# Kernel tuning notes

Measured on AMD Instinct MI355X. Metric: run time of the kernel, lower is better.

Reference implementation:

```python
import jax, jax.numpy as jnp
import numpy as np

N_NODES = 50000
N_EDGES = 640000
HIDDEN = 128
EDGE_DIM = 32


def _init_linear(key, fan_in, fan_out):
    kw, kb = jax.random.split(key)
    bound = 1.0 / np.sqrt(fan_in)
    W = jax.random.uniform(kw, (fan_in, fan_out), jnp.float32, -bound, bound)
    b = jax.random.uniform(kb, (fan_out,), jnp.float32, -bound, bound)
    return W, b


def setup_inputs() -> dict:
    key = jax.random.key(0)
    ks = jax.random.split(key, 10)
    node_features = jax.random.normal(ks[0], (N_NODES, HIDDEN), jnp.float32)
    edge_index = jax.random.randint(ks[1], (2, N_EDGES), 0, N_NODES, jnp.int64)
    edge_features = jax.random.normal(ks[2], (N_EDGES, EDGE_DIM), jnp.float32)
    coordination = jax.random.uniform(ks[3], (N_NODES,), jnp.float32)
    msg_in = 2 * HIDDEN + EDGE_DIM + 2
    upd_in = 2 * HIDDEN + 1
    mW1, mb1 = _init_linear(ks[4], msg_in, HIDDEN)
    mW2, mb2 = _init_linear(ks[5], HIDDEN, HIDDEN)
    uW1, ub1 = _init_linear(ks[6], upd_in, HIDDEN)
    uW2, ub2 = _init_linear(ks[7], HIDDEN, HIDDEN)
    ln_gamma = jnp.ones((HIDDEN,), jnp.float32)
    ln_beta = jnp.zeros((HIDDEN,), jnp.float32)
    return {
        "node_features": node_features,
        "edge_index": edge_index,
        "edge_features": edge_features,
        "coordination": coordination,
        "mW1": mW1, "mb1": mb1, "mW2": mW2, "mb2": mb2,
        "uW1": uW1, "ub1": ub1, "uW2": uW2, "ub2": ub2,
        "ln_gamma": ln_gamma, "ln_beta": ln_beta,
    }


def _layernorm(x, gamma, beta, eps=1e-5):
    mu = jnp.mean(x, axis=-1, keepdims=True)
    var = jnp.mean(jnp.square(x - mu), axis=-1, keepdims=True)
    return (x - mu) * jax.lax.rsqrt(var + eps) * gamma + beta


def reference(node_features, edge_index, edge_features, coordination,
              mW1, mb1, mW2, mb2, uW1, ub1, uW2, ub2, ln_gamma, ln_beta):
    n_nodes = node_features.shape[0]
    src, dst = edge_index[0], edge_index[1]
    # edge_input: [E, 2H + edge_dim + 2]
    edge_input = jnp.concatenate([
        node_features[src],
        node_features[dst],
        edge_features,
        coordination[src][:, None],
        coordination[dst][:, None],
    ], axis=-1)
    h = jax.nn.silu(edge_input @ mW1 + mb1)
    messages = h @ mW2 + mb2  # [E, H]
    aggregated = jax.ops.segment_sum(messages, dst, num_segments=n_nodes)  # [N, H]
    update_input = jnp.concatenate([
        node_features, aggregated, coordination[:, None]
    ], axis=-1)  # [N, 2H+1]
    u = jax.nn.silu(update_input @ uW1 + ub1)
    upd = u @ uW2 + ub2
    return _layernorm(node_features + upd, ln_gamma, ln_beta)
```

## Files before the change

### kernel.cpp

```cpp
#include <hip/hip_runtime.h>

#define NN 50000
#define NE 640000
#define HID 128


typedef __attribute__((ext_vector_type(8))) short bf8;
typedef __attribute__((ext_vector_type(4))) float f4;

#define MFMA(a, b, c) __builtin_amdgcn_mfma_f32_16x16x32_bf16(a, b, c, 0, 0, 0)

__device__ __forceinline__ short f2bf(float f) {
    union { float f; unsigned u; } v; v.f = f;
    unsigned r = v.u + 0x7FFFu + ((v.u >> 16) & 1u);
    return (short)(r >> 16);
}
__device__ __forceinline__ float bf2f(short s) {
    union { unsigned u; float f; } v; v.u = ((unsigned)(unsigned short)s) << 16;
    return v.f;
}
__device__ __forceinline__ float silu(float x) {
    return x * __builtin_amdgcn_rcpf(1.f + __expf(-x));
}

__global__ void pack_weights_kernel(const float* __restrict__ mW1, const float* __restrict__ mb1,
                                    const float* __restrict__ mW2,
                                    const float* __restrict__ uW1, const float* __restrict__ uW2,
                                    short* __restrict__ Wpre, short* __restrict__ W1e,
                                    short* __restrict__ W2p, short* __restrict__ U1p,
                                    short* __restrict__ U2p,
                                    float* __restrict__ Waux, float* __restrict__ Baux) {
    const int stride = gridDim.x * blockDim.x;
    const int idx = blockIdx.x * blockDim.x + threadIdx.x;
    for (int t = idx; t < 256 * 128; t += stride) {
        int cc = t / 128, k = t % 128;
        float v = (cc < 128) ? mW1[k * 128 + cc] : mW1[(128 + k) * 128 + (cc - 128)];
        Wpre[t] = f2bf(v);
    }
    for (int t = idx; t < 128 * 32; t += stride) {
        int c = t / 32, k = t % 32;
        W1e[t] = f2bf(mW1[(256 + k) * 128 + c]);
    }
    for (int t = idx; t < 128 * 128; t += stride)
        W2p[t] = f2bf(mW2[(t % 128) * 128 + (t / 128)]);
    for (int t = idx; t < 128 * 288; t += stride) {
        int n = t / 288, k = t % 288;
        U1p[t] = (k < 257) ? f2bf(uW1[k * 128 + n]) : (short)0;
    }
    for (int t = idx; t < 128 * 128; t += stride)
        U2p[t] = f2bf(uW2[(t % 128) * 128 + (t / 128)]);
    for (int t = idx; t < 256; t += stride) {
        Waux[t] = (t < 128) ? mW1[288 * 128 + t] : mW1[289 * 128 + (t - 128)];
        Baux[t] = (t < 128) ? 0.f : mb1[t - 128];
    }
}

__global__ __launch_bounds__(256, 3)
void node_pre_kernel(const float* __restrict__ nf, const float* __restrict__ coord,
                     const short* __restrict__ Wpre, const float* __restrict__ Waux,
                     const float* __restrict__ Baux, short* __restrict__ Ppre) {
    __shared__ short SH[64 * 264];
    __shared__ float scoord[64];
    short* A = SH;
    short* P = SH;
    const int tid = threadIdx.x;
    const int nbase = blockIdx.x * 64;

    {
        const int r = tid >> 2, q = tid & 3;
        const int node = nbase + r;
        short* Ar = A + r * 136 + q * 32;
        if (node < NN) {
            const float* p = nf + (long)node * HID + q * 32;
#pragma unroll
            for (int j = 0; j < 4; ++j) {
                f4 v0 = *(const f4*)(p + j * 8), v1 = *(const f4*)(p + j * 8 + 4);
                bf8 w = { f2bf(v0[0]), f2bf(v0[1]), f2bf(v0[2]), f2bf(v0[3]),
                          f2bf(v1[0]), f2bf(v1[1]), f2bf(v1[2]), f2bf(v1[3]) };
                *(bf8*)(Ar + j * 8) = w;
            }
            if (q == 0) scoord[r] = coord[node];
        } else {
            bf8 z = {};
#pragma unroll
            for (int j = 0; j < 4; ++j) *(bf8*)(Ar + j * 8) = z;
            if (q == 0) scoord[r] = 0.f;
        }
    }
    __syncthreads();

    const int lane = tid & 63, wv = tid >> 6;
    const int g = lane >> 4, i16 = lane & 15, wc = wv * 64;

    f4 acc[4][4] = {};
#pragma unroll
    for (int ks = 0; ks < 4; ++ks) {
        const int kb = ks * 32 + g * 8;
        bf8 b[4];
#pragma unroll
        for (int n = 0; n < 4; ++n)
            b[n] = *(const bf8*)(Wpre + (wc + n * 16 + i16) * 128 + kb);
#pragma unroll
        for (int m = 0; m < 4; ++m) {
            bf8 a = *(const bf8*)(A + (m * 16 + i16) * 136 + kb);
#pragma unroll
            for (int n = 0; n < 4; ++n) acc[m][n] = MFMA(a, b[n], acc[m][n]);
        }
    }
    __syncthreads();

#pragma unroll
    for (int n = 0; n < 4; ++n) {
        const int cc = wc + n * 16 + i16;
        const float wa = Waux[cc], ba = Baux[cc];
#pragma unroll
        for (int m = 0; m < 4; ++m)
#pragma unroll
            for (int i = 0; i < 4; ++i) {
                const int row = m * 16 + g * 4 + i;
                P[row * 264 + cc] = f2bf(acc[m][n][i] + scoord[row] * wa + ba);
            }
    }
    __syncthreads();

    {
        const int r = tid >> 2, q = tid & 3;
        const int node = nbase + r;
        if (node < NN) {
#pragma unroll
            for (int j = 0; j < 8; ++j)
                *(bf8*)(Ppre + (long)node * 256 + q * 64 + j * 8) =
                    *(const bf8*)(P + r * 264 + q * 64 + j * 8);
        }
    }
}

__global__ void hist_kernel(const int* __restrict__ ei, int* __restrict__ hist) {
    const int stride = gridDim.x * blockDim.x;
    for (int e = blockIdx.x * blockDim.x + threadIdx.x; e < NE; e += stride)
        atomicAdd(&hist[ei[NE + e]], 1);
}

__global__ void scan1_kernel(const int* __restrict__ hist, int* __restrict__ pos,
                             int* __restrict__ csum) {
    __shared__ int s[256];
    const int b = blockIdx.x, t = threadIdx.x;
    const int idx = b * 200 + t;
    int v = (t < 200) ? hist[idx] : 0;
    s[t] = v;
    __syncthreads();
    for (int d = 1; d < 256; d <<= 1) {
        int x = (t >= d) ? s[t - d] : 0;
        __syncthreads();
        s[t] += x;
        __syncthreads();
    }
    if (t < 200) pos[idx] = s[t] - v;
    if (t == 255) csum[b] = s[255];
}

__global__ void scan2_kernel(int* __restrict__ csum) {
    __shared__ int s[256];
    const int t = threadIdx.x;
    int v = (t < 250) ? csum[t] : 0;
    s[t] = v;
    __syncthreads();
    for (int d = 1; d < 256; d <<= 1) {
        int x = (t >= d) ? s[t - d] : 0;
        __syncthreads();
        s[t] += x;
        __syncthreads();
    }
    if (t < 250) csum[t] = s[t] - v;
}

__global__ void scan3_kernel(int* __restrict__ pos, const int* __restrict__ csum) {
    const int b = blockIdx.x, t = threadIdx.x;
    if (t < 200) pos[b * 200 + t] += csum[b];
}

__global__ void scatter_kernel(const int* __restrict__ ei, int* __restrict__ pos,
                               int* __restrict__ perm) {
    const int stride = gridDim.x * blockDim.x;
    for (int e = blockIdx.x * blockDim.x + threadIdx.x; e < NE; e += stride) {
        const int d = ei[NE + e];
        const int p = atomicAdd(&pos[d], 1);
        perm[p] = e;
    }
}

__global__ __launch_bounds__(256, 4)
void edge_kernel(const int* __restrict__ ei, const float* __restrict__ ef,
                 const int* __restrict__ perm, const short* __restrict__ Ppre,
                 const short* __restrict__ W1e, const short* __restrict__ W2p,
                 const float* __restrict__ mb2, float* __restrict__ agg) {
    constexpr int LDEF = 40, LDH = 136, LDM = 132;
    __shared__ float R[64 * 132];
    __shared__ int sdst[64], ssrc[64];
    short* Aef = (short*)R;
    short* H = (short*)R;
    float* M = R;

    const int tid = threadIdx.x;
    const int bid = blockIdx.x;
    const int ebase = ((bid & 7) * 1250 + (bid >> 3)) * 64;

    {
        const int r = tid >> 2, q = tid & 3;
        const int e = perm[ebase + r];
        if (q == 0) { ssrc[r] = ei[e]; sdst[r] = ei[NE + e]; }
        const float* pe = ef + (long)e * 32 + q * 8;
        f4 v0 = *(const f4*)pe, v1 = *(const f4*)(pe + 4);
        bf8 w = { f2bf(v0[0]), f2bf(v0[1]), f2bf(v0[2]), f2bf(v0[3]),
                  f2bf(v1[0]), f2bf(v1[1]), f2bf(v1[2]), f2bf(v1[3]) };
        *(bf8*)(Aef + r * LDEF + q * 8) = w;
    }
    __syncthreads();

    const int lane = tid & 63, wv = tid >> 6;
    const int g = lane >> 4, i16 = lane & 15, wc = wv * 32;

    f4 acc[4][2] = {};
    {
        bf8 b0 = *(const bf8*)(W1e + (wc + i16) * 32 + g * 8);
        bf8 b1 = *(const bf8*)(W1e + (wc + 16 + i16) * 32 + g * 8);
#pragma unroll
        for (int m = 0; m < 4; ++m) {
            bf8 a = *(const bf8*)(Aef + (m * 16 + i16) * LDEF + g * 8);
            acc[m][0] = MFMA(a, b0, acc[m][0]);
            acc[m][1] = MFMA(a, b1, acc[m][1]);
        }
    }
    __syncthreads();

#pragma unroll
    for (int m = 0; m < 4; ++m)
#pragma unroll
        for (int n = 0; n < 2; ++n)
#pragma unroll
            for (int i = 0; i < 4; ++i)
                H[(m * 16 + g * 4 + i) * LDH + wc + n * 16 + i16] = f2bf(acc[m][n][i]);
    __syncthreads();

    {
        const int r = tid >> 2, q = tid & 3;
        const short* p1 = Ppre + (long)ssrc[r] * 256 + q * 32;
        const short* p2 = Ppre + (long)sdst[r] * 256 + 128 + q * 32;
        bf8 a1[4], a2[4];
#pragma unroll
        for (int j = 0; j < 4; ++j) { a1[j] = *(const bf8*)(p1 + j * 8); }
#pragma unroll
        for (int j = 0; j < 4; ++j) { a2[j] = *(const bf8*)(p2 + j * 8); }
        short* Hr = H + r * LDH + q * 32;
#pragma unroll
        for (int j = 0; j < 4; ++j)
#pragma unroll
            for (int t = 0; t < 8; ++t) {
                float x = bf2f(Hr[j * 8 + t]) + bf2f(a1[j][t]) + bf2f(a2[j][t]);
                Hr[j * 8 + t] = f2bf(silu(x));
            }
    }
    __syncthreads();

    f4 acc2[4][2] = {};
#pragma unroll
    for (int ks = 0; ks < 4; ++ks) {
        const int kb = ks * 32 + g * 8;
        bf8 b0 = *(const bf8*)(W2p + (wc + i16) * 128 + kb);
        bf8 b1 = *(const bf8*)(W2p + (wc + 16 + i16) * 128 + kb);
#pragma unroll
        for (int m = 0; m < 4; ++m) {
            bf8 a = *(const bf8*)(H + (m * 16 + i16) * LDH + kb);
            acc2[m][0] = MFMA(a, b0, acc2[m][0]);
            acc2[m][1] = MFMA(a, b1, acc2[m][1]);
        }
    }
    __syncthreads();

    {
        const float c0 = mb2[wc + i16], c1 = mb2[wc + 16 + i16];
#pragma unroll
        for (int m = 0; m < 4; ++m)
#pragma unroll
            for (int n = 0; n < 2; ++n)
#pragma unroll
                for (int i = 0; i < 4; ++i)
                    M[(m * 16 + g * 4 + i) * LDM + wc + n * 16 + i16] =
                        acc2[m][n][i] + (n ? c1 : c0);
    }
    __syncthreads();

    {
        const int col = tid >> 1, half = tid & 1;
        const int r0 = half * 32, r1 = r0 + 32;
        float run = 0.f;
#pragma unroll
        for (int r = r0; r < r1; ++r) {
            run += M[r * LDM + col];
            const bool last = (r == r1 - 1) || (sdst[r + 1] != sdst[r]);
            if (last) {
                atomicAdd(agg + (long)sdst[r] * HID + col, run);
                run = 0.f;
            }
        }
    }
}

__global__ __launch_bounds__(256, 4)
void node_kernel(const float* __restrict__ nf, const float* __restrict__ agg,
                 const float* __restrict__ coord,
                 const short* __restrict__ U1p, const float* __restrict__ ub1,
                 const short* __restrict__ U2p, const float* __restrict__ ub2,
                 const float* __restrict__ gamma, const float* __restrict__ beta,
                 float* __restrict__ out) {
    constexpr int K1 = 288, LDA = 296, LDH = 136, LDX = 132;
    __shared__ short SH[64 * LDA];
    short* A = SH;
    short* H = SH;
    float* X = (float*)SH;

    const int tid = threadIdx.x;
    const int nbase = blockIdx.x * 64;

    {
        const int r = tid >> 2, q = tid & 3;
        const int node = nbase + r;
        short* Ar = A + r * LDA;
        bf8 z = {};
        if (node < NN) {
            const float* pn = nf + (long)node * HID + q * 32;
            const float* pa = agg + (long)node * HID + q * 32;
#pragma unroll
            for (int j = 0; j < 4; ++j) {
                f4 v0 = *(const f4*)(pn + j * 8), v1 = *(const f4*)(pn + j * 8 + 4);
                bf8 w = { f2bf(v0[0]), f2bf(v0[1]), f2bf(v0[2]), f2bf(v0[3]),
                          f2bf(v1[0]), f2bf(v1[1]), f2bf(v1[2]), f2bf(v1[3]) };
                *(bf8*)(Ar + q * 32 + j * 8) = w;
            }
#pragma unroll
            for (int j = 0; j < 4; ++j) {
                f4 v0 = *(const f4*)(pa + j * 8), v1 = *(const f4*)(pa + j * 8 + 4);
                bf8 w = { f2bf(v0[0]), f2bf(v0[1]), f2bf(v0[2]), f2bf(v0[3]),
                          f2bf(v1[0]), f2bf(v1[1]), f2bf(v1[2]), f2bf(v1[3]) };
                *(bf8*)(Ar + 128 + q * 32 + j * 8) = w;
            }
            *(bf8*)(Ar + 256 + q * 8) = z;
            if (q == 0) Ar[256] = f2bf(coord[node]);
        } else {
#pragma unroll
            for (int j = 0; j < 4; ++j) {
                *(bf8*)(Ar + q * 32 + j * 8) = z;
                *(bf8*)(Ar + 128 + q * 32 + j * 8) = z;
            }
            *(bf8*)(Ar + 256 + q * 8) = z;
        }
    }
    __syncthreads();

    const int lane = tid & 63, wv = tid >> 6;
    const int g = lane >> 4, i16 = lane & 15, wc = wv * 32;

    f4 acc[4][2] = {};
#pragma unroll
    for (int ks = 0; ks < K1 / 32; ++ks) {
        const int kb = ks * 32 + g * 8;
        bf8 b0 = *(const bf8*)(U1p + (wc + i16) * K1 + kb);
        bf8 b1 = *(const bf8*)(U1p + (wc + 16 + i16) * K1 + kb);
#pragma unroll
        for (int m = 0; m < 4; ++m) {
            bf8 a = *(const bf8*)(A + (m * 16 + i16) * LDA + kb);
            acc[m][0] = MFMA(a, b0, acc[m][0]);
            acc[m][1] = MFMA(a, b1, acc[m][1]);
        }
    }
    __syncthreads();

    {
        const float c0 = ub1[wc + i16], c1 = ub1[wc + 16 + i16];
#pragma unroll
        for (int m = 0; m < 4; ++m)
#pragma unroll
            for (int n = 0; n < 2; ++n)
#pragma unroll
                for (int i = 0; i < 4; ++i) {
                    float x = acc[m][n][i] + (n ? c1 : c0);
                    H[(m * 16 + g * 4 + i) * LDH + wc + n * 16 + i16] = f2bf(silu(x));
                }
    }
    __syncthreads();

    f4 acc2[4][2] = {};
#pragma unroll
    for (int ks = 0; ks < 4; ++ks) {
        const int kb = ks * 32 + g * 8;
        bf8 b0 = *(const bf8*)(U2p + (wc + i16) * 128 + kb);
        bf8 b1 = *(const bf8*)(U2p + (wc + 16 + i16) * 128 + kb);
#pragma unroll
        for (int m = 0; m < 4; ++m) {
            bf8 a = *(const bf8*)(H + (m * 16 + i16) * LDH + kb);
            acc2[m][0] = MFMA(a, b0, acc2[m][0]);
            acc2[m][1] = MFMA(a, b1, acc2[m][1]);
        }
    }
    __syncthreads();

    {
        const float c0 = ub2[wc + i16], c1 = ub2[wc + 16 + i16];
#pragma unroll
        for (int m = 0; m < 4; ++m)
#pragma unroll
            for (int n = 0; n < 2; ++n)
#pragma unroll
                for (int i = 0; i < 4; ++i) {
                    const int row = m * 16 + g * 4 + i;
                    const int node = nbase + row;
                    const int col = wc + n * 16 + i16;
                    float v = acc2[m][n][i] + (n ? c1 : c0);
                    float base = (node < NN) ? nf[(long)node * HID + col] : 0.f;
                    X[row * LDX + col] = base + v;
                }
    }
    __syncthreads();

    {
        const int r = tid >> 2, q = tid & 3;
        const int node = nbase + r;
        float s = 0.f;
#pragma unroll
        for (int j = 0; j < 32; ++j) s += X[r * LDX + q * 32 + j];
        s += __shfl_xor(s, 1);
        s += __shfl_xor(s, 2);
        const float mu = s * (1.f / 128.f);
        float vv = 0.f;
#pragma unroll
        for (int j = 0; j < 32; ++j) {
            float d = X[r * LDX + q * 32 + j] - mu;
            vv += d * d;
        }
        vv += __shfl_xor(vv, 1);
        vv += __shfl_xor(vv, 2);
        const float rstd = rsqrtf(vv * (1.f / 128.f) + 1e-5f);
        if (node < NN) {
#pragma unroll
            for (int j = 0; j < 32; ++j) {
                const int c = q * 32 + j;
                out[(long)node * HID + c] = (X[r * LDX + c] - mu) * rstd * gamma[c] + beta[c];
            }
        }
    }
}

extern "C" void kernel_launch(void* const* d_in, const int* in_sizes, int n_in,
                              void* d_out, int out_size, void* d_ws, size_t ws_size,
                              hipStream_t stream) {
    const float* nf    = (const float*)d_in[0];
    const int*   ei    = (const int*)d_in[1];
    const float* ef    = (const float*)d_in[2];
    const float* coord = (const float*)d_in[3];
    const float* mW1 = (const float*)d_in[4];
    const float* mb1 = (const float*)d_in[5];
    const float* mW2 = (const float*)d_in[6];
    const float* mb2 = (const float*)d_in[7];
    const float* uW1 = (const float*)d_in[8];
    const float* ub1 = (const float*)d_in[9];
    const float* uW2 = (const float*)d_in[10];
    const float* ub2 = (const float*)d_in[11];
    const float* gamma = (const float*)d_in[12];
    const float* beta  = (const float*)d_in[13];
    float* out = (float*)d_out;

    char* ws = (char*)d_ws;
    float* agg  = (float*)ws;
    short* Wpre = (short*)(ws + 25600000);
    short* W1e  = (short*)(ws + 25665536);
    short* W2p  = (short*)(ws + 25673728);
    short* U1p  = (short*)(ws + 25706496);
    short* U2p  = (short*)(ws + 25780224);
    float* Waux = (float*)(ws + 25812992);
    float* Baux = (float*)(ws + 25814016);
    int* hist = (int*)(ws + 25815040);
    int* pos  = (int*)(ws + 26015040);
    int* csum = (int*)(ws + 26215040);
    int* perm = (int*)(ws + 26216064);
    short* Ppre = (short*)d_out;

    hipMemsetAsync(agg, 0, (size_t)NN * HID * sizeof(float), stream);
    hipMemsetAsync(hist, 0, (size_t)NN * sizeof(int), stream);
    pack_weights_kernel<<<64, 256, 0, stream>>>(mW1, mb1, mW2, uW1, uW2,
                                                Wpre, W1e, W2p, U1p, U2p, Waux, Baux);
    node_pre_kernel<<<(NN + 63) / 64, 256, 0, stream>>>(nf, coord, Wpre, Waux, Baux, Ppre);
    hist_kernel<<<1024, 256, 0, stream>>>(ei, hist);
    scan1_kernel<<<250, 256, 0, stream>>>(hist, pos, csum);
    scan2_kernel<<<1, 256, 0, stream>>>(csum);
    scan3_kernel<<<250, 256, 0, stream>>>(pos, csum);
    scatter_kernel<<<1024, 256, 0, stream>>>(ei, pos, perm);
    edge_kernel<<<NE / 64, 256, 0, stream>>>(ei, ef, perm, Ppre, W1e, W2p, mb2, agg);
    node_kernel<<<(NN + 63) / 64, 256, 0, stream>>>(nf, agg, coord,
                                                    U1p, ub1, U2p, ub2, gamma, beta, out);
}
```

Before: 262.9 us.

## Hoist gathers ahead of first GEMM and restructure edge kernel LDS usage

Issues the W1e fragment, bias, edge-feature, src/dst index and Ppre row gathers at kernel entry so their global latency overlaps the edge-feature staging and first MFMA. Separates the edge-feature buffer from the H/M buffer, which removes one barrier, and pads the H stride. It also vectorises the SiLU read-modify-write into bf8 LDS accesses and remaps the segmented-reduction threads so consecutive lanes cover consecutive columns. The cost is higher register pressure from holding the gathered rows across the first GEMM, and slightly more LDS per block.

```diff
diff --git a/kernel.cpp b/kernel.cpp
--- a/kernel.cpp
+++ b/kernel.cpp
@@ -194,10 +194,10 @@
                  const int* __restrict__ perm, const short* __restrict__ Ppre,
                  const short* __restrict__ W1e, const short* __restrict__ W2p,
                  const float* __restrict__ mb2, float* __restrict__ agg) {
-    constexpr int LDEF = 40, LDH = 136, LDM = 132;
-    __shared__ float R[64 * 132];
-    __shared__ int sdst[64], ssrc[64];
-    short* Aef = (short*)R;
+    constexpr int LDEF = 40, LDH = 140, LDM = 132;
+    __shared__ short Aef[64 * LDEF];
+    __shared__ float R[64 * LDM];
+    __shared__ int sdst[64];
     short* H = (short*)R;
     float* M = R;
 
@@ -205,60 +205,64 @@
     const int bid = blockIdx.x;
     const int ebase = ((bid & 7) * 1250 + (bid >> 3)) * 64;
 
-    {
-        const int r = tid >> 2, q = tid & 3;
-        const int e = perm[ebase + r];
-        if (q == 0) { ssrc[r] = ei[e]; sdst[r] = ei[NE + e]; }
-        const float* pe = ef + (long)e * 32 + q * 8;
-        f4 v0 = *(const f4*)pe, v1 = *(const f4*)(pe + 4);
+    const int lane = tid & 63, wv = tid >> 6;
+    const int g = lane >> 4, i16 = lane & 15, wc = wv * 32;
+    const int r = tid >> 2, q = tid & 3;
+
+    bf8 b0 = *(const bf8*)(W1e + (wc + i16) * 32 + g * 8);
+    bf8 b1 = *(const bf8*)(W1e + (wc + 16 + i16) * 32 + g * 8);
+    const float c0 = mb2[wc + i16], c1 = mb2[wc + 16 + i16];
+    const int e = perm[ebase + r];
+    const float* pe = ef + (long)e * 32 + q * 8;
+    f4 v0 = *(const f4*)pe, v1 = *(const f4*)(pe + 4);
+    const int s = ei[e];
+    const int d = ei[NE + e];
+    const short* p1 = Ppre + (long)s * 256 + q * 32;
+    const short* p2 = Ppre + (long)d * 256 + 128 + q * 32;
+    bf8 a1[4], a2[4];
+#pragma unroll
+    for (int j = 0; j < 4; ++j) a1[j] = *(const bf8*)(p1 + j * 8);
+#pragma unroll
+    for (int j = 0; j < 4; ++j) a2[j] = *(const bf8*)(p2 + j * 8);
+    if (q == 0) sdst[r] = d;
+    {
         bf8 w = { f2bf(v0[0]), f2bf(v0[1]), f2bf(v0[2]), f2bf(v0[3]),
                   f2bf(v1[0]), f2bf(v1[1]), f2bf(v1[2]), f2bf(v1[3]) };
         *(bf8*)(Aef + r * LDEF + q * 8) = w;
     }
     __syncthreads();
 
-    const int lane = tid & 63, wv = tid >> 6;
-    const int g = lane >> 4, i16 = lane & 15, wc = wv * 32;
-
-    f4 acc[4][2] = {};
-    {
-        bf8 b0 = *(const bf8*)(W1e + (wc + i16) * 32 + g * 8);
-        bf8 b1 = *(const bf8*)(W1e + (wc + 16 + i16) * 32 + g * 8);
+    {
+        f4 acc[4][2] = {};
 #pragma unroll
         for (int m = 0; m < 4; ++m) {
             bf8 a = *(const bf8*)(Aef + (m * 16 + i16) * LDEF + g * 8);
             acc[m][0] = MFMA(a, b0, acc[m][0]);
             acc[m][1] = MFMA(a, b1, acc[m][1]);
         }
-    }
-    __syncthreads();
-
-#pragma unroll
-    for (int m = 0; m < 4; ++m)
-#pragma unroll
-        for (int n = 0; n < 2; ++n)
-#pragma unroll
-            for (int i = 0; i < 4; ++i)
-                H[(m * 16 + g * 4 + i) * LDH + wc + n * 16 + i16] = f2bf(acc[m][n][i]);
-    __syncthreads();
-
-    {
-        const int r = tid >> 2, q = tid & 3;
-        const short* p1 = Ppre + (long)ssrc[r] * 256 + q * 32;
-        const short* p2 = Ppre + (long)sdst[r] * 256 + 128 + q * 32;
-        bf8 a1[4], a2[4];
-#pragma unroll
-        for (int j = 0; j < 4; ++j) { a1[j] = *(const bf8*)(p1 + j * 8); }
-#pragma unroll
-        for (int j = 0; j < 4; ++j) { a2[j] = *(const bf8*)(p2 + j * 8); }
+#pragma unroll
+        for (int m = 0; m < 4; ++m)
+#pragma unroll
+            for (int n = 0; n < 2; ++n)
+#pragma unroll
+                for (int i = 0; i < 4; ++i)
+                    H[(m * 16 + g * 4 + i) * LDH + wc + n * 16 + i16] = f2bf(acc[m][n][i]);
+    }
+    __syncthreads();
+
+    {
         short* Hr = H + r * LDH + q * 32;
 #pragma unroll
-        for (int j = 0; j < 4; ++j)
+        for (int j = 0; j < 4; ++j) {
+            bf8 hv = *(const bf8*)(Hr + j * 8);
+            bf8 o;
 #pragma unroll
             for (int t = 0; t < 8; ++t) {
-                float x = bf2f(Hr[j * 8 + t]) + bf2f(a1[j][t]) + bf2f(a2[j][t]);
-                Hr[j * 8 + t] = f2bf(silu(x));
-            }
+                float x = bf2f(hv[t]) + bf2f(a1[j][t]) + bf2f(a2[j][t]);
+                o[t] = f2bf(silu(x));
+            }
+            *(bf8*)(Hr + j * 8) = o;
+        }
     }
     __syncthreads();
 
@@ -266,19 +270,18 @@
 #pragma unroll
     for (int ks = 0; ks < 4; ++ks) {
         const int kb = ks * 32 + g * 8;
-        bf8 b0 = *(const bf8*)(W2p + (wc + i16) * 128 + kb);
-        bf8 b1 = *(const bf8*)(W2p + (wc + 16 + i16) * 128 + kb);
+        bf8 w0 = *(const bf8*)(W2p + (wc + i16) * 128 + kb);
+        bf8 w1 = *(const bf8*)(W2p + (wc + 16 + i16) * 128 + kb);
 #pragma unroll
         for (int m = 0; m < 4; ++m) {
             bf8 a = *(const bf8*)(H + (m * 16 + i16) * LDH + kb);
-            acc2[m][0] = MFMA(a, b0, acc2[m][0]);
-            acc2[m][1] = MFMA(a, b1, acc2[m][1]);
-        }
-    }
-    __syncthreads();
-
-    {
-        const float c0 = mb2[wc + i16], c1 = mb2[wc + 16 + i16];
+            acc2[m][0] = MFMA(a, w0, acc2[m][0]);
+            acc2[m][1] = MFMA(a, w1, acc2[m][1]);
+        }
+    }
+    __syncthreads();
+
+    {
 #pragma unroll
         for (int m = 0; m < 4; ++m)
 #pragma unroll
@@ -291,15 +294,16 @@
     __syncthreads();
 
     {
-        const int col = tid >> 1, half = tid & 1;
-        const int r0 = half * 32, r1 = r0 + 32;
+        const int col = tid & 127, half = tid >> 7;
+        const int r0 = half * 32;
         float run = 0.f;
 #pragma unroll
-        for (int r = r0; r < r1; ++r) {
-            run += M[r * LDM + col];
-            const bool last = (r == r1 - 1) || (sdst[r + 1] != sdst[r]);
+        for (int rr = 0; rr < 32; ++rr) {
+            const int row = r0 + rr;
+            run += M[row * LDM + col];
+            const bool last = (rr == 31) || (sdst[row + 1] != sdst[row]);
             if (last) {
-                atomicAdd(agg + (long)sdst[r] * HID + col, run);
+                atomicAdd(agg + (long)sdst[row] * HID + col, run);
                 run = 0.f;
             }
         }
```

Result: slower. 308.1 us (+17.2%).
